# Optimization experiments

Measured on AMD Instinct MI355X. Metric: run time of the kernel, lower is better.

## Reference

```python
import jax, jax.numpy as jnp
import numpy as np

N_FREQ = 50          # n_frequencies
ENC_DIM = N_FREQ * 4 # sine encoding output dim = 200
EMB = 10             # n_embedding_dimensions
N_FRAG = 1_000_000
CELLS = 500
GENES = 500


def setup_inputs() -> dict:
    key = jax.random.key(0)
    ks = jax.random.split(key, 12)
    coordinates = jax.random.normal(ks[0], (N_FRAG, 2), jnp.float32) * 1000.0
    fragment_cellxgene_ix = jnp.sort(
        jax.random.randint(ks[1], (N_FRAG,), 0, CELLS * GENES, dtype=jnp.int32))
    # FragmentEmbedder MLP: Linear(200,10) -> Sigmoid -> Linear(10,10)
    W1 = jax.random.normal(ks[2], (ENC_DIM, EMB), jnp.float32) * 0.07
    b1 = jnp.zeros((EMB,), jnp.float32)
    W2 = jax.random.normal(ks[3], (EMB, EMB), jnp.float32) * 0.3
    b2 = jnp.zeros((EMB,), jnp.float32)
    # EmbeddingToExpression MLP: Linear(10,10) -> Sigmoid -> Linear(10,1)
    We1 = jax.random.normal(ks[4], (EMB, EMB), jnp.float32) * 0.3
    be1 = jnp.zeros((EMB,), jnp.float32)
    We2 = jax.random.normal(ks[5], (EMB, 1), jnp.float32) * 0.3
    be2 = jnp.zeros((1,), jnp.float32)
    return dict(coordinates=coordinates, fragment_cellxgene_ix=fragment_cellxgene_ix,
                cell_n=CELLS, gene_n=GENES,
                W1=W1, b1=b1, W2=W2, b2=b2, We1=We1, be1=be1, We2=We2, be2=be2)


def _sine_encode(coordinates):
    # frequencies: [1/1000**(2i/nf)]*2 for i in 1..nf, flattened -> [2*nf]
    i = jnp.arange(1, N_FREQ + 1, dtype=jnp.float32)
    freqs = jnp.repeat(1.0 / 1000.0 ** (2.0 * i / N_FREQ), 2)          # [100]
    shifts = jnp.tile(jnp.array([0.0, np.pi / 2], jnp.float32), N_FREQ)  # [100]
    # coordinates [N,2] -> [N,2,100] -> [N,400]? No: flatten(-2) over last two dims -> [N, 2*100]=[N,200]
    phase = coordinates[..., None] * freqs + shifts                     # [N,2,100]
    return jnp.sin(phase.reshape(coordinates.shape[0], -1))             # [N,200]


def reference(coordinates, fragment_cellxgene_ix, cell_n, gene_n,
              W1, b1, W2, b2, We1, be1, We2, be2):
    # fragment embedder
    enc = _sine_encode(coordinates)                       # [N, 200]
    h = jax.nn.sigmoid(enc @ W1 + b1)                     # [N, 10]
    emb = h @ W2 + b2                                     # [N, 10]
    # gene pooler: segment_sum over sorted cellxgene indices
    pooled = jax.ops.segment_sum(emb, fragment_cellxgene_ix,
                                 num_segments=cell_n * gene_n,
                                 indices_are_sorted=True)  # [cell*gene, 10]
    cg = pooled.reshape(cell_n, gene_n, -1)                # [cells, genes, 10]
    # embedding to expression
    h2 = jax.nn.sigmoid(cg @ We1 + be1)                    # [cells, genes, 10]
    out = (h2 @ We2 + be2)[..., 0]                         # [cells, genes]
    return out
```

## Files before the change

kernel.cpp:

```cpp
#include <hip/hip_runtime.h>
#include <hip/hip_bf16.h>

#define NFREQ 50
#define EMBD  10

typedef __attribute__((ext_vector_type(8))) short short8;
typedef __attribute__((ext_vector_type(4))) float f32x4;

__device__ __forceinline__ unsigned short bf16b(float x) {
    union { __hip_bfloat16 b; unsigned short u; } c;
    c.b = __float2bfloat16(x);
    return c.u;
}

__device__ const float C_TAB[7][4] = {
    {7.58577575029184e-1f, 5.75439937337157e-1f, 4.36515832240166e-1f, 3.31131121482591e-1f},
    {9.12010839355910e-3f, 6.91830970918936e-3f, 5.24807460249773e-3f, 3.98107170553497e-3f},
    {1.09647819614318e-4f, 8.31763771102671e-5f, 6.30957344480193e-5f, 4.78630092322638e-5f},
    {1.31825673855641e-6f, 1.00000000000000e-6f, 7.58577575029184e-7f, 5.75439937337157e-7f},
    {1.58489319246111e-8f, 1.20226443461741e-8f, 9.12010839355910e-9f, 6.91830970918936e-9f},
    {1.90546071796325e-10f,1.44543977074593e-10f,1.09647819614318e-10f,8.31763771102671e-11f},
    {2.29086765276777e-12f,1.73780082874938e-12f,1.31825673855641e-12f,1.00000000000000e-12f}
};

__device__ __forceinline__ constexpr bool lin_slot(int kt, int p) {
    return (kt == 2 && p >= 1) || (kt == 5 && p == 3) || (kt == 6);
}

__global__ void zero_ws(float4* p, int n4) {
    int t = blockIdx.x * blockDim.x + threadIdx.x;
    float4 z = make_float4(0.f, 0.f, 0.f, 0.f);
    for (int i = t; i < n4; i += gridDim.x * blockDim.x) p[i] = z;
}

__global__ __launch_bounds__(256) void frag_kernel(
    const float2* __restrict__ coords, const int* __restrict__ cgix,
    const float* __restrict__ W1, const float* __restrict__ b1,
    const float* __restrict__ W2, const float* __restrict__ b2,
    float* __restrict__ pooled, int n)
{
    __shared__ unsigned short w1lds[7 * 4 * 16 * 8];
    __shared__ float hbuf[4][64][11];
    const int tid  = threadIdx.x;
    const int wid  = tid >> 6;
    const int lane = tid & 63;
    const int grp  = lane >> 4;
    const int col  = lane & 15;
    const int t = blockIdx.x * 256 + wid * 64 + lane;
    const bool active = t < n;

    #pragma unroll
    for (int it = 0; it < 14; ++it) {
        int idx = it * 256 + tid;
        int e = idx & 7, c = (idx >> 3) & 15, g = (idx >> 7) & 3, kt = idx >> 9;
        int k = kt * 32 + g * 8 + e;
        float w = (k < 2 * NFREQ * 2 && c < EMBD) ? W1[k * EMBD + c] : 0.f;
        w1lds[idx] = bf16b(w);
    }
    __syncthreads();

    short8 Bf[7];
    #pragma unroll
    for (int kt = 0; kt < 7; ++kt)
        Bf[kt] = *reinterpret_cast<const short8*>(&w1lds[((kt * 4 + grp) * 16 + col) * 8]);

    float G = (grp == 0) ? 1.0f
            : (grp == 1) ? 3.31131121482591e-1f
            : (grp == 2) ? 1.09647819614318e-1f
                         : 3.63078054770101e-2f;
    float gi = G * 0.15915494309189535f;
    float gy = gi * 1.0e6f;

    float2 cc = active ? coords[t] : make_float2(0.f, 0.f);
    int   seg = active ? cgix[t] : -1;
    float b1v = (col < EMBD) ? b1[col] : 0.f;

    #pragma unroll
    for (int s = 0; s < 4; ++s) {
        float cx = __shfl(cc.x, s * 16 + col, 64);
        float cy = __shfl(cc.y, s * 16 + col, 64);
        float ax  = cx * gi;
        float ay  = cy * gy;
        float a01 = (grp == 0) ? ax : ay;
        f32x4 acc = {b1v, b1v, b1v, b1v};
        #pragma unroll
        for (int kt = 0; kt < 7; ++kt) {
            short8 a;
            #pragma unroll
            for (int p = 0; p < 4; ++p) {
                float base;
                if      (kt < 3) base = ax;
                else if (kt > 3) base = ay;
                else             base = (p < 2) ? a01 : ay;
                if (lin_slot(kt, p)) {
                    float phi = base * (C_TAB[kt][p] * 6.28318530717958647f);
                    float t2  = phi * phi;
                    float sv  = phi * fmaf(t2, -0.16666666666f, 1.0f);
                    float cv  = fmaf(t2, -0.5f, 1.0f);
                    if (kt == 6 && grp != 0) { sv = 0.f; cv = 0.f; }
                    a[2*p]   = (short)bf16b(sv);
                    a[2*p+1] = (short)bf16b(cv);
                } else {
                    float rr = __builtin_amdgcn_fractf(base * C_TAB[kt][p]);
                    a[2*p]   = (short)bf16b(__builtin_amdgcn_sinf(rr));
                    a[2*p+1] = (short)bf16b(__builtin_amdgcn_cosf(rr));
                }
            }
            acc = __builtin_amdgcn_mfma_f32_16x16x32_bf16(a, Bf[kt], acc, 0, 0, 0);
        }
        if (col < EMBD) {
            #pragma unroll
            for (int r = 0; r < 4; ++r)
                hbuf[wid][s * 16 + grp * 4 + r][col] = acc[r];
        }
    }
    asm volatile("s_waitcnt lgkmcnt(0)" ::: "memory");
    __builtin_amdgcn_sched_barrier(0);

    float h[EMBD];
    #pragma unroll
    for (int j = 0; j < EMBD; ++j) {
        float a = hbuf[wid][lane][j];
        h[j] = __builtin_amdgcn_rcpf(1.0f + __expf(-a));
    }
    float e[EMBD];
    #pragma unroll
    for (int j = 0; j < EMBD; ++j) e[j] = b2[j];
    #pragma unroll
    for (int m = 0; m < EMBD; ++m) {
        #pragma unroll
        for (int j = 0; j < EMBD; ++j) e[j] = fmaf(h[m], W2[m * EMBD + j], e[j]);
    }

    for (int d = 1; d < 64; d <<= 1) {
        int sup = __shfl_up(seg, d, 64);
        bool ok = (lane >= d) && (sup == seg);
        if (__builtin_amdgcn_ballot_w64(ok) == 0ull) break;
        #pragma unroll
        for (int j = 0; j < EMBD; ++j) {
            float u = __shfl_up(e[j], d, 64);
            e[j] += ok ? u : 0.0f;
        }
    }

    int seg_next = __shfl_down(seg, 1, 64);
    bool writer = active && ((lane == 63) || (seg_next != seg));
    int first_seg = __shfl(seg, 0, 64);
    int last_seg  = __shfl(seg, 63, 64);

    if (writer) {
        float* p = pooled + (long)seg * EMBD;
        if (seg == first_seg || seg == last_seg) {
            #pragma unroll
            for (int j = 0; j < EMBD; ++j) unsafeAtomicAdd(p + j, e[j]);
        } else {
            #pragma unroll
            for (int j = 0; j < EMBD; ++j) p[j] = e[j];
        }
    }
}

__global__ __launch_bounds__(256) void expr_kernel(
    const float* __restrict__ pooled,
    const float* __restrict__ We1, const float* __restrict__ be1,
    const float* __restrict__ We2, const float* __restrict__ be2,
    float* __restrict__ out, int nseg)
{
    int t = blockIdx.x * blockDim.x + threadIdx.x;
    if (t >= nseg) return;
    const float2* p2 = (const float2*)(pooled + (long)t * EMBD);
    float x[EMBD];
    #pragma unroll
    for (int j = 0; j < EMBD / 2; ++j) {
        float2 v = p2[j];
        x[2*j] = v.x; x[2*j+1] = v.y;
    }
    float o = be2[0];
    #pragma unroll
    for (int j = 0; j < EMBD; ++j) {
        float a = be1[j];
        #pragma unroll
        for (int m = 0; m < EMBD; ++m) a = fmaf(x[m], We1[m * EMBD + j], a);
        float hj = __builtin_amdgcn_rcpf(1.0f + __expf(-a));
        o = fmaf(hj, We2[j], o);
    }
    out[t] = o;
}

extern "C" void kernel_launch(void* const* d_in, const int* in_sizes, int n_in,
                              void* d_out, int out_size, void* d_ws, size_t ws_size,
                              hipStream_t stream) {
    const float2* coords = (const float2*)d_in[0];
    const int*    cgix   = (const int*)d_in[1];
    const float*  W1     = (const float*)d_in[4];
    const float*  b1     = (const float*)d_in[5];
    const float*  W2     = (const float*)d_in[6];
    const float*  b2     = (const float*)d_in[7];
    const float*  We1    = (const float*)d_in[8];
    const float*  be1    = (const float*)d_in[9];
    const float*  We2    = (const float*)d_in[10];
    const float*  be2    = (const float*)d_in[11];
    float*        out    = (float*)d_out;

    int n    = in_sizes[0] / 2;
    int nseg = out_size;
    float* pooled = (float*)d_ws;

    int n4 = (nseg * EMBD) / 4;
    int zb = (n4 + 255) / 256;
    zero_ws<<<zb, 256, 0, stream>>>((float4*)pooled, n4);

    frag_kernel<<<(n + 255) / 256, 256, 0, stream>>>(coords, cgix, W1, b1, W2, b2,
                                                     pooled, n);
    expr_kernel<<<(nseg + 255) / 256, 256, 0, stream>>>(pooled, We1, be1, We2, be2,
                                                        out, nseg);
}
```

Before: 54.84 us.

## Replace wave shuffle segmented scan with block-level LDS atomic segment pooling

Swaps the per-wave shuffle-based segmented scan for block-wide reduction. Each fragment is assigned a compacted segment slot via ballot/mbcnt across the 256-thread block, accumulated with LDS atomics, and only the block's first and last segments get global atomics. The hidden-activation buffer is also transposed so MFMA results are written as float4 and read conflict-free. This cuts shuffle work and global atomics at wave boundaries, at the cost of extra __syncthreads, LDS atomics and buffer reuse.

```diff
diff --git a/kernel.cpp b/kernel.cpp
--- a/kernel.cpp
+++ b/kernel.cpp
@@ -33,21 +33,37 @@
     for (int i = t; i < n4; i += gridDim.x * blockDim.x) p[i] = z;
 }
 
+#define SMEM_BYTES 18064
+#define HOFF 7168
+#define WOFF 18048
+
 __global__ __launch_bounds__(256) void frag_kernel(
     const float2* __restrict__ coords, const int* __restrict__ cgix,
     const float* __restrict__ W1, const float* __restrict__ b1,
     const float* __restrict__ W2, const float* __restrict__ b2,
     float* __restrict__ pooled, int n)
 {
-    __shared__ unsigned short w1lds[7 * 4 * 16 * 8];
-    __shared__ float hbuf[4][64][11];
+    __shared__ __align__(16) unsigned char smem[SMEM_BYTES];
+    unsigned short* w1lds = (unsigned short*)smem;
+    float (*hbufT)[10][68] = (float (*)[10][68])(smem + HOFF);
+    float* pool = (float*)smem;
+    int*   wcnt = (int*)(smem + WOFF);
+
     const int tid  = threadIdx.x;
     const int wid  = tid >> 6;
     const int lane = tid & 63;
     const int grp  = lane >> 4;
     const int col  = lane & 15;
-    const int t = blockIdx.x * 256 + wid * 64 + lane;
+    const int t = blockIdx.x * 256 + tid;
     const bool active = t < n;
+
+    int seg  = active ? cgix[t] : -1;
+    int segp = (active && t > 0) ? cgix[t - 1] : -2;
+    bool flag = active && ((tid == 0) || (seg != segp));
+    unsigned long long bal = __builtin_amdgcn_ballot_w64(flag);
+    int mb = __builtin_amdgcn_mbcnt_hi((unsigned)(bal >> 32),
+             __builtin_amdgcn_mbcnt_lo((unsigned)bal, 0u));
+    if (lane == 0) wcnt[wid] = __popcll(bal);
 
     #pragma unroll
     for (int it = 0; it < 14; ++it) {
@@ -72,7 +88,6 @@
     float gy = gi * 1.0e6f;
 
     float2 cc = active ? coords[t] : make_float2(0.f, 0.f);
-    int   seg = active ? cgix[t] : -1;
     float b1v = (col < EMBD) ? b1[col] : 0.f;
 
     #pragma unroll
@@ -108,11 +123,8 @@
             }
             acc = __builtin_amdgcn_mfma_f32_16x16x32_bf16(a, Bf[kt], acc, 0, 0, 0);
         }
-        if (col < EMBD) {
-            #pragma unroll
-            for (int r = 0; r < 4; ++r)
-                hbuf[wid][s * 16 + grp * 4 + r][col] = acc[r];
-        }
+        if (col < EMBD)
+            *reinterpret_cast<f32x4*>(&hbufT[wid][col][s * 16 + grp * 4]) = acc;
     }
     asm volatile("s_waitcnt lgkmcnt(0)" ::: "memory");
     __builtin_amdgcn_sched_barrier(0);
@@ -120,7 +132,7 @@
     float h[EMBD];
     #pragma unroll
     for (int j = 0; j < EMBD; ++j) {
-        float a = hbuf[wid][lane][j];
+        float a = hbufT[wid][j][lane];
         h[j] = __builtin_amdgcn_rcpf(1.0f + __expf(-a));
     }
     float e[EMBD];
@@ -132,30 +144,39 @@
         for (int j = 0; j < EMBD; ++j) e[j] = fmaf(h[m], W2[m * EMBD + j], e[j]);
     }
 
-    for (int d = 1; d < 64; d <<= 1) {
-        int sup = __shfl_up(seg, d, 64);
-        bool ok = (lane >= d) && (sup == seg);
-        if (__builtin_amdgcn_ballot_w64(ok) == 0ull) break;
-        #pragma unroll
-        for (int j = 0; j < EMBD; ++j) {
-            float u = __shfl_up(e[j], d, 64);
-            e[j] += ok ? u : 0.0f;
-        }
-    }
-
-    int seg_next = __shfl_down(seg, 1, 64);
-    bool writer = active && ((lane == 63) || (seg_next != seg));
-    int first_seg = __shfl(seg, 0, 64);
-    int last_seg  = __shfl(seg, 63, 64);
-
-    if (writer) {
-        float* p = pooled + (long)seg * EMBD;
-        if (seg == first_seg || seg == last_seg) {
+    __syncthreads();
+    {
+        float4 z4 = make_float4(0.f, 0.f, 0.f, 0.f);
+        float* pz = pool + tid * EMBD;
+        *reinterpret_cast<float2*>(pz)     = make_float2(0.f, 0.f);
+        *reinterpret_cast<float4*>(pz + 2) = z4;
+        *reinterpret_cast<float4*>(pz + 6) = z4;
+    }
+    __syncthreads();
+
+    int woff = 0;
+    #pragma unroll
+    for (int wv = 0; wv < 4; ++wv) woff += (wv < wid) ? wcnt[wv] : 0;
+    int tot = wcnt[0] + wcnt[1] + wcnt[2] + wcnt[3];
+    int slot = woff + mb + (flag ? 0 : -1);
+
+    if (active) {
+        float* pb = pool + slot * EMBD;
+        #pragma unroll
+        for (int j = 0; j < EMBD; ++j) atomicAdd(pb + j, e[j]);
+    }
+    __syncthreads();
+
+    if (flag) {
+        const float* pb = pool + slot * EMBD;
+        float* g = pooled + (long)seg * EMBD;
+        bool bdry = (slot == 0) || (slot == tot - 1);
+        if (bdry) {
             #pragma unroll
-            for (int j = 0; j < EMBD; ++j) unsafeAtomicAdd(p + j, e[j]);
+            for (int j = 0; j < EMBD; ++j) unsafeAtomicAdd(g + j, pb[j]);
         } else {
             #pragma unroll
-            for (int j = 0; j < EMBD; ++j) p[j] = e[j];
+            for (int j = 0; j < EMBD; ++j) g[j] = pb[j];
         }
     }
 }
```

Result: slower. 111.2 us (+102.8%).
